# Performance work log

Measured on AMD Instinct MI355X. Metric: run time of the kernel, lower is better.

The kernel has to match this reference:

```python
import jax, jax.numpy as jnp
import numpy as np

B, S, H, NH, NL, G, D, A, T = 32, 512, 512, 8, 6, 8, 256, 18, 1024
HD = H // NH


def setup_inputs() -> dict:
    key = jax.random.key(0)
    ks = jax.random.split(key, 32)
    def n(k, shape, s=0.02):
        return jax.random.normal(k, shape, jnp.float32) * s
    return {
        'game_indices': jax.random.randint(ks[0], (B,), 0, G),
        'states': jax.random.normal(ks[1], (B, S, D), jnp.float32),
        'actions': jax.random.randint(ks[2], (B, S), 0, A),
        'returns_to_go': jax.random.normal(ks[3], (B, S), jnp.float32),
        'timesteps': jax.random.randint(ks[4], (B, S), 0, T),
        'attention_mask': jnp.ones((B, S), jnp.int32),
        'game_emb': n(ks[5], (G, H)),
        'obs_W': n(ks[6], (G, D, H)),
        'obs_b': n(ks[7], (G, H)),
        'obs_ln_g': jnp.ones((G, H), jnp.float32),
        'obs_ln_b': jnp.zeros((G, H), jnp.float32),
        'act_emb': n(ks[8], (G, A, H)),
        'ret_W': n(ks[9], (H,)),
        'ret_b': n(ks[10], (H,)),
        'time_emb': n(ks[11], (T, H)),
        'Wqkv': n(ks[12], (NL, 3 * H, H)),
        'bqkv': n(ks[13], (NL, 3 * H)),
        'Wo': n(ks[14], (NL, H, H)),
        'bo': n(ks[15], (NL, H)),
        'ln1_g': jnp.ones((NL, H), jnp.float32),
        'ln1_b': jnp.zeros((NL, H), jnp.float32),
        'W1': n(ks[16], (NL, 4 * H, H)),
        'b1': n(ks[17], (NL, 4 * H)),
        'W2': n(ks[18], (NL, H, 4 * H)),
        'b2': n(ks[19], (NL, H)),
        'ln2_g': jnp.ones((NL, H), jnp.float32),
        'ln2_b': jnp.zeros((NL, H), jnp.float32),
        'sh_W': n(ks[20], (G, H, D)),
        'sh_b': n(ks[21], (G, D)),
        'ah_W': n(ks[22], (G, H, A)),
        'ah_b': n(ks[23], (G, A)),
        'rh_W': n(ks[24], (H, 1)),
        'rh_b': n(ks[25], (1,)),
    }


def _ln(x, g, b, eps=1e-5):
    m = jnp.mean(x, -1, keepdims=True)
    v = jnp.mean((x - m) ** 2, -1, keepdims=True)
    return (x - m) / jnp.sqrt(v + eps) * g + b


def reference(game_indices, states, actions, returns_to_go, timesteps, attention_mask,
              game_emb, obs_W, obs_b, obs_ln_g, obs_ln_b, act_emb, ret_W, ret_b, time_emb,
              Wqkv, bqkv, Wo, bo, ln1_g, ln1_b, W1, b1, W2, b2, ln2_g, ln2_b,
              sh_W, sh_b, ah_W, ah_b, rh_W, rh_b):
    gi = game_indices
    g_emb = game_emb[gi][:, None, :]  # [B,1,H]
    # per-game routed observation embedding: Linear -> LayerNorm -> ReLU (grouped GEMM by game)
    se = jnp.einsum('bsd,bdh->bsh', states, obs_W[gi]) + obs_b[gi][:, None, :]
    se = jax.nn.relu(_ln(se, obs_ln_g[gi][:, None, :], obs_ln_b[gi][:, None, :]))
    # per-game routed action embedding table lookup
    ae = act_emb[gi[:, None], actions]  # [B,S,H]
    re = returns_to_go[..., None] * ret_W + ret_b  # Linear(1,H)
    te = time_emb[timesteps]
    x = se + ae + re + te + g_emb
    # key padding mask (src_key_padding_mask: True where attention_mask==0)
    bias = jnp.where((attention_mask == 0)[:, None, None, :], -1e9, 0.0)  # [B,1,1,S]
    scale = 1.0 / jnp.sqrt(jnp.asarray(HD, jnp.float32))
    for l in range(NL):  # post-norm TransformerEncoderLayer, relu, dropout=0 (eval)
        qkv = jnp.einsum('bsh,oh->bso', x, Wqkv[l]) + bqkv[l]
        q, k, v = jnp.split(qkv, 3, axis=-1)
        q = q.reshape(B, S, NH, HD).transpose(0, 2, 1, 3)
        k = k.reshape(B, S, NH, HD).transpose(0, 2, 1, 3)
        v = v.reshape(B, S, NH, HD).transpose(0, 2, 1, 3)
        scores = jnp.einsum('bhqd,bhkd->bhqk', q, k) * scale + bias
        attn = jnp.einsum('bhqk,bhkd->bhqd', jax.nn.softmax(scores, -1), v)
        attn = attn.transpose(0, 2, 1, 3).reshape(B, S, H)
        attn = jnp.einsum('bsh,oh->bso', attn, Wo[l]) + bo[l]
        x = _ln(x + attn, ln1_g[l], ln1_b[l])
        ff = jax.nn.relu(jnp.einsum('bsh,fh->bsf', x, W1[l]) + b1[l])
        ff = jnp.einsum('bsf,hf->bsh', ff, W2[l]) + b2[l]
        x = _ln(x + ff, ln2_g[l], ln2_b[l])
    # per-game routed prediction heads
    state_preds = jnp.einsum('bsh,bho->bso', x, sh_W[gi]) + sh_b[gi][:, None, :]
    action_preds = jnp.einsum('bsh,bho->bso', x, ah_W[gi]) + ah_b[gi][:, None, :]
    return_preds = x @ rh_W + rh_b
    return (state_preds, action_preds, return_preds)
```

## Files before the change

kernel.cpp:

```cpp
#include <hip/hip_runtime.h>

typedef __bf16 bf16x4 __attribute__((ext_vector_type(4)));
typedef __bf16 bf16x8 __attribute__((ext_vector_type(8)));
typedef float f32x4 __attribute__((ext_vector_type(4)));
typedef int int4v __attribute__((ext_vector_type(4)));

#define LOG2E 1.44269504088896340736f

typedef const __attribute__((address_space(1))) void gvoid_t;
typedef __attribute__((address_space(3))) void lvoid_t;


__global__ void cvt_f32_bf16(const float* __restrict__ src, __bf16* __restrict__ dst, int n4)
{
    int i = blockIdx.x * blockDim.x + threadIdx.x;
    if (i >= n4) return;
    f32x4 v = *reinterpret_cast<const f32x4*>(src + (size_t)i * 4);
    bf16x4 o;
    #pragma unroll
    for (int k = 0; k < 4; ++k) o[k] = (__bf16)v[k];
    *reinterpret_cast<bf16x4*>(dst + (size_t)i * 4) = o;
}

__global__ void transpose_cvt(const float* __restrict__ src, __bf16* __restrict__ dst, int R, int C)
{
    int m = blockIdx.y;
    int n = R * C;
    int i = blockIdx.x * 256 + threadIdx.x;
    if (i >= n) return;
    int c = i / R, r = i - c * R;
    dst[(size_t)m * n + i] = (__bf16)src[(size_t)m * n + (size_t)r * C + c];
}

__global__ void transpose_f32(const float* __restrict__ src, float* __restrict__ dst, int R, int C)
{
    int m = blockIdx.y;
    int n = R * C;
    int i = blockIdx.x * 256 + threadIdx.x;
    if (i >= n) return;
    int c = i / R, r = i - c * R;
    dst[(size_t)m * n + i] = src[(size_t)m * n + (size_t)r * C + c];
}

__global__ __launch_bounds__(256, 2)
void gemm_bt(const __bf16* __restrict__ A, size_t strideA,
             const __bf16* __restrict__ B, size_t strideB,
             const float* __restrict__ bias, int strideBias,
             float* Cf, __bf16* Cb, size_t strideC,
             const int* __restrict__ gidx,
             int K, int ldc, int relu)
{
    __shared__ __align__(16) char smem[16384];
    __bf16* lA  = (__bf16*)smem;
    __bf16* lB  = (__bf16*)(smem + 8192);
    __bf16* lCb = (__bf16*)smem;
    float*  lCf = (float*)smem;

    const int z = blockIdx.z;
    const int g = gidx ? gidx[z] : 0;
    const __bf16* Ab = A + (size_t)z * strideA;
    const __bf16* Bb = B + (size_t)g * strideB;

    const int nx = gridDim.x;
    const int nwg = nx * gridDim.y;
    int orig = blockIdx.y * nx + blockIdx.x;
    int wg = ((nwg & 7) == 0) ? ((orig & 7) * (nwg >> 3) + (orig >> 3)) : orig;
    const int bm = (wg / nx) * 128, bn = (wg % nx) * 128;

    const int t = threadIdx.x;
    const int w = t >> 6, lane = t & 63;
    const int wr = (w >> 1) * 64, wc = (w & 1) * 64;
    const int l16 = lane & 15, lk = lane >> 4;

    const int srow = lane >> 2;
    const int schunk = (lane & 3) ^ (srow & 3);
    const int ca = (lk ^ (l16 & 3)) * 8;

    f32x4 acc[4][4] = {};

    for (int kt = 0; kt < K; kt += 32) {
        __syncthreads();
        #pragma unroll
        for (int jj = 0; jj < 2; ++jj) {
            const __bf16* ga = Ab + (size_t)(bm + w * 32 + jj * 16 + srow) * K + kt + schunk * 8;
            __builtin_amdgcn_global_load_lds((gvoid_t*)ga, (lvoid_t*)&lA[(w * 32 + jj * 16) * 32], 16, 0, 0);
            const __bf16* gb = Bb + (size_t)(bn + w * 32 + jj * 16 + srow) * K + kt + schunk * 8;
            __builtin_amdgcn_global_load_lds((gvoid_t*)gb, (lvoid_t*)&lB[(w * 32 + jj * 16) * 32], 16, 0, 0);
        }
        __syncthreads();

        bf16x8 af[4], bfr[4];
        #pragma unroll
        for (int i = 0; i < 4; ++i) {
            af[i]  = *reinterpret_cast<const bf16x8*>(&lA[(wr + i * 16 + l16) * 32 + ca]);
            bfr[i] = *reinterpret_cast<const bf16x8*>(&lB[(wc + i * 16 + l16) * 32 + ca]);
        }
        #pragma unroll
        for (int mi = 0; mi < 4; ++mi)
            #pragma unroll
            for (int ni = 0; ni < 4; ++ni)
                acc[mi][ni] = __builtin_amdgcn_mfma_f32_16x16x32_bf16(af[mi], bfr[ni], acc[mi][ni], 0, 0, 0);
    }

    const float* biasb = bias ? bias + (size_t)g * strideBias : nullptr;

    if (Cb) {
        #pragma unroll
        for (int p = 0; p < 2; ++p) {
            __syncthreads();
            if (wr == p * 64) {
                #pragma unroll
                for (int ni = 0; ni < 4; ++ni) {
                    int col = wc + ni * 16 + l16;
                    float bv = biasb ? biasb[bn + col] : 0.f;
                    #pragma unroll
                    for (int mi = 0; mi < 4; ++mi)
                        #pragma unroll
                        for (int j = 0; j < 4; ++j) {
                            float v = acc[mi][ni][j] + bv;
                            if (relu) v = fmaxf(v, 0.f);
                            lCb[(mi * 16 + lk * 4 + j) * 128 + col] = (__bf16)v;
                        }
                }
            }
            __syncthreads();
            #pragma unroll
            for (int it = 0; it < 4; ++it) {
                int off = it * 2048 + t * 8;
                int rl = off >> 7, col = off & 127;
                *reinterpret_cast<int4v*>(Cb + (size_t)z * strideC + (size_t)(bm + p * 64 + rl) * ldc + bn + col) =
                    *reinterpret_cast<const int4v*>(&lCb[off]);
            }
        }
    } else {
        #pragma unroll
        for (int p = 0; p < 4; ++p) {
            __syncthreads();
            #pragma unroll
            for (int mi = 0; mi < 4; ++mi) {
                int rl = wr + mi * 16;
                if (rl >= p * 32 && rl < p * 32 + 32) {
                    #pragma unroll
                    for (int ni = 0; ni < 4; ++ni) {
                        int col = wc + ni * 16 + l16;
                        float bv = biasb ? biasb[bn + col] : 0.f;
                        #pragma unroll
                        for (int j = 0; j < 4; ++j) {
                            float v = acc[mi][ni][j] + bv;
                            if (relu) v = fmaxf(v, 0.f);
                            lCf[(rl - p * 32 + lk * 4 + j) * 128 + col] = v;
                        }
                    }
                }
            }
            __syncthreads();
            #pragma unroll
            for (int it = 0; it < 4; ++it) {
                int off = it * 1024 + t * 4;
                int rl = off >> 7, col = off & 127;
                *reinterpret_cast<f32x4*>(Cf + (size_t)z * strideC + (size_t)(bm + p * 32 + rl) * ldc + bn + col) =
                    *reinterpret_cast<const f32x4*>(&lCf[off]);
            }
        }
    }
}

__global__ __launch_bounds__(256, 2)
void attn_fwd(const __bf16* __restrict__ qkv, const int* __restrict__ mask,
              __bf16* __restrict__ out)
{
    __shared__ __bf16 lQ[128 * 64];
    __shared__ __bf16 lK[128 * 64];
    __shared__ __bf16 lVt[64 * 128];
    __shared__ float lMask[128];
    __shared__ __bf16 lP[4][32 * 32];

    const int b = blockIdx.z, h = blockIdx.y, q0 = blockIdx.x * 128;
    const int t = threadIdx.x, w = t >> 6, lane = t & 63;
    const int l16 = lane & 15, lk = lane >> 4;

    const __bf16* qbase = qkv + (size_t)b * 512 * 1536 + h * 64;
    const __bf16* kbase = qbase + 512;
    const __bf16* vbase = qbase + 1024;

    #pragma unroll
    for (int r = 0; r < 4; ++r) {
        int c = t + r * 256;
        int row = c >> 3, ch = c & 7;
        *reinterpret_cast<int4v*>(&lQ[row * 64 + ((ch ^ (row & 7)) * 8)]) =
            *reinterpret_cast<const int4v*>(qbase + (size_t)(q0 + row) * 1536 + ch * 8);
    }

    float m_run[2][4], l_run[2][4];
    f32x4 oacc[2][4] = {};
    #pragma unroll
    for (int mi = 0; mi < 2; ++mi)
        #pragma unroll
        for (int j = 0; j < 4; ++j) { m_run[mi][j] = -1e30f; l_run[mi][j] = 0.f; }

    for (int kt = 0; kt < 512; kt += 128) {
        __syncthreads();
        #pragma unroll
        for (int r = 0; r < 4; ++r) {
            int c = t + r * 256;
            int row = c >> 3, ch = c & 7;
            *reinterpret_cast<int4v*>(&lK[row * 64 + ((ch ^ (row & 7)) * 8)]) =
                *reinterpret_cast<const int4v*>(kbase + (size_t)(kt + row) * 1536 + ch * 8);
        }
        #pragma unroll
        for (int r = 0; r < 4; ++r) {
            int c = t + r * 256;
            int d = c & 63, kc8 = c >> 6;
            bf16x8 vv;
            #pragma unroll
            for (int i = 0; i < 8; ++i)
                vv[i] = vbase[(size_t)(kt + kc8 * 8 + i) * 1536 + d];
            *reinterpret_cast<bf16x8*>(&lVt[d * 128 + ((kc8 ^ (d & 7)) * 8)]) = vv;
        }
        if (t < 128) lMask[t] = (mask[b * 512 + kt + t] == 0) ? -1e9f : 0.f;
        __syncthreads();

        f32x4 sacc[2][8] = {};
        #pragma unroll
        for (int kc = 0; kc < 2; ++kc) {
            bf16x8 qf[2], kf[8];
            #pragma unroll
            for (int mi = 0; mi < 2; ++mi) {
                int row = w * 32 + mi * 16 + l16;
                qf[mi] = *reinterpret_cast<const bf16x8*>(&lQ[row * 64 + (((kc * 4 + lk) ^ (row & 7)) * 8)]);
            }
            #pragma unroll
            for (int ni = 0; ni < 8; ++ni) {
                int row = ni * 16 + l16;
                kf[ni] = *reinterpret_cast<const bf16x8*>(&lK[row * 64 + (((kc * 4 + lk) ^ (row & 7)) * 8)]);
            }
            #pragma unroll
            for (int mi = 0; mi < 2; ++mi)
                #pragma unroll
                for (int ni = 0; ni < 8; ++ni)
                    sacc[mi][ni] = __builtin_amdgcn_mfma_f32_16x16x32_bf16(qf[mi], kf[ni], sacc[mi][ni], 0, 0, 0);
        }

        #pragma unroll
        for (int mi = 0; mi < 2; ++mi) {
            float alpha[4];
            #pragma unroll
            for (int j = 0; j < 4; ++j) {
                float mx = -1e30f;
                #pragma unroll
                for (int ni = 0; ni < 8; ++ni) {
                    float sv = sacc[mi][ni][j] * 0.125f + lMask[ni * 16 + l16];
                    sacc[mi][ni][j] = sv;
                    mx = fmaxf(mx, sv);
                }
                #pragma unroll
                for (int d = 8; d >= 1; d >>= 1) mx = fmaxf(mx, __shfl_xor(mx, d));
                float mn = fmaxf(m_run[mi][j], mx);
                alpha[j] = exp2f((m_run[mi][j] - mn) * LOG2E);
                m_run[mi][j] = mn;
                float ps = 0.f;
                #pragma unroll
                for (int ni = 0; ni < 8; ++ni) {
                    float p = exp2f((sacc[mi][ni][j] - mn) * LOG2E);
                    sacc[mi][ni][j] = p;
                    ps += p;
                }
                l_run[mi][j] = l_run[mi][j] * alpha[j] + ps;
            }
            #pragma unroll
            for (int dn = 0; dn < 4; ++dn)
                #pragma unroll
                for (int j = 0; j < 4; ++j)
                    oacc[mi][dn][j] *= alpha[j];
        }

        __bf16* lp = &lP[w][0];
        #pragma unroll
        for (int kc = 0; kc < 4; ++kc) {
            #pragma unroll
            for (int mi = 0; mi < 2; ++mi)
                #pragma unroll
                for (int n2 = 0; n2 < 2; ++n2)
                    #pragma unroll
                    for (int j = 0; j < 4; ++j) {
                        int row = mi * 16 + lk * 4 + j;
                        lp[row * 32 + n2 * 16 + l16] = (__bf16)sacc[mi][kc * 2 + n2][j];
                    }
            bf16x8 pf[2], vf[4];
            #pragma unroll
            for (int mi = 0; mi < 2; ++mi)
                pf[mi] = *reinterpret_cast<const bf16x8*>(&lp[(mi * 16 + l16) * 32 + lk * 8]);
            #pragma unroll
            for (int dn = 0; dn < 4; ++dn) {
                int d = dn * 16 + l16;
                vf[dn] = *reinterpret_cast<const bf16x8*>(&lVt[d * 128 + (((kc * 4 + lk) ^ (d & 7)) * 8)]);
            }
            #pragma unroll
            for (int mi = 0; mi < 2; ++mi)
                #pragma unroll
                for (int dn = 0; dn < 4; ++dn)
                    oacc[mi][dn] = __builtin_amdgcn_mfma_f32_16x16x32_bf16(pf[mi], vf[dn], oacc[mi][dn], 0, 0, 0);
        }
    }

    #pragma unroll
    for (int mi = 0; mi < 2; ++mi) {
        float linv[4];
        #pragma unroll
        for (int j = 0; j < 4; ++j) {
            float s = l_run[mi][j];
            #pragma unroll
            for (int d = 8; d >= 1; d >>= 1) s += __shfl_xor(s, d);
            linv[j] = 1.f / s;
        }
        #pragma unroll
        for (int dn = 0; dn < 4; ++dn)
            #pragma unroll
            for (int j = 0; j < 4; ++j) {
                int row = q0 + w * 32 + mi * 16 + lk * 4 + j;
                int col = h * 64 + dn * 16 + l16;
                out[(size_t)(b * 512 + row) * 512 + col] = (__bf16)(oacc[mi][dn][j] * linv[j]);
            }
    }
}


__device__ __forceinline__ float wsum64(float v)
{
    #pragma unroll
    for (int d = 32; d >= 1; d >>= 1) v += __shfl_xor(v, d);
    return v;
}

__global__ __launch_bounds__(256)
void ln_fuse(const float* resid, const __bf16* __restrict__ proj,
             const float* __restrict__ gamma, const float* __restrict__ beta,
             float* xfo, __bf16* __restrict__ xbo)
{
    int tok = blockIdx.x * 4 + (threadIdx.x >> 6);
    int lane = threadIdx.x & 63;
    size_t base = (size_t)tok * 512 + lane * 8;
    float y[8];
    {
        f32x4 a0 = *reinterpret_cast<const f32x4*>(resid + base);
        f32x4 a1 = *reinterpret_cast<const f32x4*>(resid + base + 4);
        bf16x8 pv = *reinterpret_cast<const bf16x8*>(proj + base);
        #pragma unroll
        for (int i = 0; i < 4; ++i) { y[i] = a0[i] + (float)pv[i]; y[4 + i] = a1[i] + (float)pv[4 + i]; }
    }
    float s = 0.f;
    #pragma unroll
    for (int i = 0; i < 8; ++i) s += y[i];
    float mean = wsum64(s) * (1.f / 512.f);
    float v = 0.f;
    #pragma unroll
    for (int i = 0; i < 8; ++i) { float d = y[i] - mean; v += d * d; }
    float rstd = rsqrtf(wsum64(v) * (1.f / 512.f) + 1e-5f);
    int hh = lane * 8;
    f32x4 g0 = *reinterpret_cast<const f32x4*>(gamma + hh);
    f32x4 g1 = *reinterpret_cast<const f32x4*>(gamma + hh + 4);
    f32x4 b0 = *reinterpret_cast<const f32x4*>(beta + hh);
    f32x4 b1 = *reinterpret_cast<const f32x4*>(beta + hh + 4);
    f32x4 o0, o1;
    bf16x8 ob;
    #pragma unroll
    for (int i = 0; i < 4; ++i) {
        float t0 = (y[i] - mean) * rstd * g0[i] + b0[i];
        float t1 = (y[4 + i] - mean) * rstd * g1[i] + b1[i];
        o0[i] = t0; o1[i] = t1;
        ob[i] = (__bf16)t0; ob[4 + i] = (__bf16)t1;
    }
    *reinterpret_cast<f32x4*>(xfo + base) = o0;
    *reinterpret_cast<f32x4*>(xfo + base + 4) = o1;
    *reinterpret_cast<bf16x8*>(xbo + base) = ob;
}

__global__ __launch_bounds__(256)
void embed_fin(const __bf16* __restrict__ seraw, const int* __restrict__ gi,
               const int* __restrict__ actions, const float* __restrict__ rtg,
               const int* __restrict__ ts,
               const float* __restrict__ olg, const float* __restrict__ olb,
               const float* __restrict__ act_emb, const float* __restrict__ retW,
               const float* __restrict__ retb, const float* __restrict__ time_emb,
               const float* __restrict__ game_emb,
               float* __restrict__ xfo, __bf16* __restrict__ xbo)
{
    int tok = blockIdx.x * 4 + (threadIdx.x >> 6);
    int lane = threadIdx.x & 63;
    int b = tok >> 9;
    int g = gi[b];
    int a = actions[tok];
    int tt = ts[tok];
    float rv = rtg[tok];
    size_t base = (size_t)tok * 512 + lane * 8;
    int hh = lane * 8;

    float y[8];
    {
        bf16x8 a0 = *reinterpret_cast<const bf16x8*>(seraw + base);
        #pragma unroll
        for (int i = 0; i < 8; ++i) y[i] = (float)a0[i];
    }
    float s = 0.f;
    #pragma unroll
    for (int i = 0; i < 8; ++i) s += y[i];
    float mean = wsum64(s) * (1.f / 512.f);
    float v = 0.f;
    #pragma unroll
    for (int i = 0; i < 8; ++i) { float d = y[i] - mean; v += d * d; }
    float rstd = rsqrtf(wsum64(v) * (1.f / 512.f) + 1e-5f);

    const float* gp = olg + (size_t)g * 512 + hh;
    const float* bp = olb + (size_t)g * 512 + hh;
    const float* ap = act_emb + ((size_t)g * 18 + a) * 512 + hh;
    const float* tp = time_emb + (size_t)tt * 512 + hh;
    const float* ep = game_emb + (size_t)g * 512 + hh;
    const float* rwp = retW + hh;
    const float* rbp = retb + hh;

    f32x4 o0, o1;
    bf16x8 ob;
    #pragma unroll
    for (int half = 0; half < 2; ++half) {
        f32x4 gv = *reinterpret_cast<const f32x4*>(gp + half * 4);
        f32x4 bv = *reinterpret_cast<const f32x4*>(bp + half * 4);
        f32x4 av = *reinterpret_cast<const f32x4*>(ap + half * 4);
        f32x4 tv = *reinterpret_cast<const f32x4*>(tp + half * 4);
        f32x4 ev = *reinterpret_cast<const f32x4*>(ep + half * 4);
        f32x4 rw = *reinterpret_cast<const f32x4*>(rwp + half * 4);
        f32x4 rb = *reinterpret_cast<const f32x4*>(rbp + half * 4);
        #pragma unroll
        for (int i = 0; i < 4; ++i) {
            float n = (y[half * 4 + i] - mean) * rstd * gv[i] + bv[i];
            n = fmaxf(n, 0.f);
            float o = n + av[i] + rv * rw[i] + rb[i] + tv[i] + ev[i];
            if (half == 0) o0[i] = o; else o1[i] = o;
            ob[half * 4 + i] = (__bf16)o;
        }
    }
    *reinterpret_cast<f32x4*>(xfo + base) = o0;
    *reinterpret_cast<f32x4*>(xfo + base + 4) = o1;
    *reinterpret_cast<bf16x8*>(xbo + base) = ob;
}

__global__ __launch_bounds__(256)
void head_ar(const float* __restrict__ xf, const int* __restrict__ gi,
             const float* __restrict__ ahWt, const float* __restrict__ ah_b,
             const float* __restrict__ rhW, const float* __restrict__ rhb,
             float* __restrict__ outA, float* __restrict__ outR)
{
    int tok = blockIdx.x * 4 + (threadIdx.x >> 6);
    int lane = threadIdx.x & 63;
    int b = tok >> 9;
    int g = gi[b];
    size_t base = (size_t)tok * 512 + lane * 8;
    float x[8];
    {
        f32x4 a0 = *reinterpret_cast<const f32x4*>(xf + base);
        f32x4 a1 = *reinterpret_cast<const f32x4*>(xf + base + 4);
        #pragma unroll
        for (int i = 0; i < 4; ++i) { x[i] = a0[i]; x[4 + i] = a1[i]; }
    }
    #pragma unroll 1
    for (int a = 0; a < 18; ++a) {
        const float* wp = ahWt + ((size_t)g * 18 + a) * 512 + lane * 8;
        f32x4 w0 = *reinterpret_cast<const f32x4*>(wp);
        f32x4 w1 = *reinterpret_cast<const f32x4*>(wp + 4);
        float p = 0.f;
        #pragma unroll
        for (int i = 0; i < 4; ++i) { p += x[i] * w0[i]; p += x[4 + i] * w1[i]; }
        p = wsum64(p);
        if (lane == 0) outA[(size_t)tok * 18 + a] = p + ah_b[g * 18 + a];
    }
    {
        const float* wp = rhW + lane * 8;
        f32x4 w0 = *reinterpret_cast<const f32x4*>(wp);
        f32x4 w1 = *reinterpret_cast<const f32x4*>(wp + 4);
        float p = 0.f;
        #pragma unroll
        for (int i = 0; i < 4; ++i) { p += x[i] * w0[i]; p += x[4 + i] * w1[i]; }
        p = wsum64(p);
        if (lane == 0) outR[tok] = p + rhb[0];
    }
}


extern "C" void kernel_launch(void* const* d_in, const int* in_sizes, int n_in,
                              void* d_out, int out_size, void* d_ws, size_t ws_size,
                              hipStream_t stream)
{
    (void)in_sizes; (void)n_in; (void)out_size; (void)ws_size;

    const int*   gi       = (const int*)d_in[0];
    const float* states   = (const float*)d_in[1];
    const int*   actions  = (const int*)d_in[2];
    const float* rtg      = (const float*)d_in[3];
    const int*   ts       = (const int*)d_in[4];
    const int*   amask    = (const int*)d_in[5];
    const float* game_emb = (const float*)d_in[6];
    const float* obs_W    = (const float*)d_in[7];
    const float* obs_b    = (const float*)d_in[8];
    const float* obs_ln_g = (const float*)d_in[9];
    const float* obs_ln_b = (const float*)d_in[10];
    const float* act_emb  = (const float*)d_in[11];
    const float* ret_W    = (const float*)d_in[12];
    const float* ret_b    = (const float*)d_in[13];
    const float* time_emb = (const float*)d_in[14];
    const float* Wqkv     = (const float*)d_in[15];
    const float* bqkv     = (const float*)d_in[16];
    const float* Wo       = (const float*)d_in[17];
    const float* bo       = (const float*)d_in[18];
    const float* ln1_g    = (const float*)d_in[19];
    const float* ln1_b    = (const float*)d_in[20];
    const float* W1       = (const float*)d_in[21];
    const float* b1       = (const float*)d_in[22];
    const float* W2       = (const float*)d_in[23];
    const float* b2       = (const float*)d_in[24];
    const float* ln2_g    = (const float*)d_in[25];
    const float* ln2_b    = (const float*)d_in[26];
    const float* sh_W     = (const float*)d_in[27];
    const float* sh_b     = (const float*)d_in[28];
    const float* ah_W     = (const float*)d_in[29];
    const float* ah_b     = (const float*)d_in[30];
    const float* rh_W     = (const float*)d_in[31];
    const float* rh_b     = (const float*)d_in[32];

    char* wsb = (char*)d_ws;
    float*  xf      = (float*)(wsb + 0);
    __bf16* xb      = (__bf16*)(wsb + 33554432);
    __bf16* tmp     = (__bf16*)(wsb + 50331648);
    __bf16* qkvB    = (__bf16*)(wsb + 83886080);
    __bf16* ff1B    = qkvB;
    __bf16* statesB = qkvB;
    __bf16* obswB   = (__bf16*)(wsb + 83886080 + 8388608);
    __bf16* attnB   = (__bf16*)(wsb + 150994944);
    __bf16* wqkvB   = (__bf16*)(wsb + 167772160);
    __bf16* woB     = (__bf16*)(wsb + 177209344);
    __bf16* w1B     = (__bf16*)(wsb + 180355072);
    __bf16* w2B     = (__bf16*)(wsb + 192937984);
    __bf16* shwB    = (__bf16*)(wsb + 205520896);
    float*  ahwT    = (float*)(wsb + 207618048);

    cvt_f32_bf16<<<4608, 256, 0, stream>>>(Wqkv, wqkvB, 1179648);
    cvt_f32_bf16<<<1536, 256, 0, stream>>>(Wo, woB, 393216);
    cvt_f32_bf16<<<6144, 256, 0, stream>>>(W1, w1B, 1572864);
    cvt_f32_bf16<<<6144, 256, 0, stream>>>(W2, w2B, 1572864);
    cvt_f32_bf16<<<4096, 256, 0, stream>>>(states, statesB, 1048576);
    transpose_cvt<<<dim3(512, 8), 256, 0, stream>>>(obs_W, obswB, 256, 512);
    transpose_cvt<<<dim3(512, 8), 256, 0, stream>>>(sh_W, shwB, 512, 256);
    transpose_f32<<<dim3(36, 8), 256, 0, stream>>>(ah_W, ahwT, 512, 18);

    gemm_bt<<<dim3(4, 4, 32), 256, 0, stream>>>(
        statesB, (size_t)512 * 256, obswB, (size_t)512 * 256, obs_b, 512,
        nullptr, tmp, (size_t)512 * 512, gi, 256, 512, 0);
    embed_fin<<<4096, 256, 0, stream>>>(tmp, gi, actions, rtg, ts,
        obs_ln_g, obs_ln_b, act_emb, ret_W, ret_b, time_emb, game_emb, xf, xb);

    for (int l = 0; l < 6; ++l) {
        gemm_bt<<<dim3(12, 128, 1), 256, 0, stream>>>(
            xb, 0, wqkvB + (size_t)l * 1536 * 512, 0, bqkv + l * 1536, 0,
            nullptr, qkvB, 0, nullptr, 512, 1536, 0);
        attn_fwd<<<dim3(4, 8, 32), 256, 0, stream>>>(qkvB, amask, attnB);
        gemm_bt<<<dim3(4, 128, 1), 256, 0, stream>>>(
            attnB, 0, woB + (size_t)l * 512 * 512, 0, bo + l * 512, 0,
            nullptr, tmp, 0, nullptr, 512, 512, 0);
        ln_fuse<<<4096, 256, 0, stream>>>(xf, tmp, ln1_g + l * 512, ln1_b + l * 512, xf, xb);
        gemm_bt<<<dim3(16, 128, 1), 256, 0, stream>>>(
            xb, 0, w1B + (size_t)l * 2048 * 512, 0, b1 + l * 2048, 0,
            nullptr, ff1B, 0, nullptr, 512, 2048, 1);
        gemm_bt<<<dim3(4, 128, 1), 256, 0, stream>>>(
            ff1B, 0, w2B + (size_t)l * 512 * 2048, 0, b2 + l * 512, 0,
            nullptr, tmp, 0, nullptr, 2048, 512, 0);
        ln_fuse<<<4096, 256, 0, stream>>>(xf, tmp, ln2_g + l * 512, ln2_b + l * 512, xf, xb);
    }

    gemm_bt<<<dim3(2, 4, 32), 256, 0, stream>>>(
        xb, (size_t)512 * 512, shwB, (size_t)256 * 512, sh_b, 256,
        (float*)d_out, nullptr, (size_t)512 * 256, gi, 512, 256, 0);
    head_ar<<<4096, 256, 0, stream>>>(xf, gi, ahwT, ah_b, rh_W, rh_b,
        (float*)d_out + 4194304, (float*)d_out + 4489216);
}
```

Measured before the change: 1.635 ms.

## Double-buffer GEMM LDS tiles, keep Q in registers, skip unneeded softmax rescales

The GEMM now double-buffers its A/B LDS tiles so the next k-slice loads while MFMAs run, drops one barrier per iteration, and writes the output tile in fewer epilogue passes using the larger LDS. Occupancy hints go up for both kernels. The attention kernel keeps Q fragments in registers instead of LDS and folds scale times log2e into one FMA. It also skips the running-max rescale when no lane's max changed and swizzles the P scratch layout to cut bank conflicts. The costs are more LDS per GEMM block, which may conflict with the higher occupancy target, and more register pressure in attention.

```diff
diff --git a/kernel.cpp b/kernel.cpp
--- a/kernel.cpp
+++ b/kernel.cpp
@@ -6,6 +6,7 @@
 typedef int int4v __attribute__((ext_vector_type(4)));
 
 #define LOG2E 1.44269504088896340736f
+#define C1SM  0.18033688011112042592f
 
 typedef const __attribute__((address_space(1))) void gvoid_t;
 typedef __attribute__((address_space(3))) void lvoid_t;
@@ -42,7 +43,7 @@
     dst[(size_t)m * n + i] = src[(size_t)m * n + (size_t)r * C + c];
 }
 
-__global__ __launch_bounds__(256, 2)
+__global__ __launch_bounds__(256, 4)
 void gemm_bt(const __bf16* __restrict__ A, size_t strideA,
              const __bf16* __restrict__ B, size_t strideB,
              const float* __restrict__ bias, int strideBias,
@@ -50,9 +51,7 @@
              const int* __restrict__ gidx,
              int K, int ldc, int relu)
 {
-    __shared__ __align__(16) char smem[16384];
-    __bf16* lA  = (__bf16*)smem;
-    __bf16* lB  = (__bf16*)(smem + 8192);
+    __shared__ __align__(16) char smem[32768];
     __bf16* lCb = (__bf16*)smem;
     float*  lCf = (float*)smem;
 
@@ -78,36 +77,68 @@
 
     f32x4 acc[4][4] = {};
 
-    for (int kt = 0; kt < K; kt += 32) {
-        __syncthreads();
+    auto stage = [&](int buf, int kt) {
+        __bf16* la = (__bf16*)(smem + buf * 16384);
+        __bf16* lb = la + 4096;
         #pragma unroll
         for (int jj = 0; jj < 2; ++jj) {
             const __bf16* ga = Ab + (size_t)(bm + w * 32 + jj * 16 + srow) * K + kt + schunk * 8;
-            __builtin_amdgcn_global_load_lds((gvoid_t*)ga, (lvoid_t*)&lA[(w * 32 + jj * 16) * 32], 16, 0, 0);
+            __builtin_amdgcn_global_load_lds((gvoid_t*)ga, (lvoid_t*)&la[(w * 32 + jj * 16) * 32], 16, 0, 0);
             const __bf16* gb = Bb + (size_t)(bn + w * 32 + jj * 16 + srow) * K + kt + schunk * 8;
-            __builtin_amdgcn_global_load_lds((gvoid_t*)gb, (lvoid_t*)&lB[(w * 32 + jj * 16) * 32], 16, 0, 0);
-        }
-        __syncthreads();
-
+            __builtin_amdgcn_global_load_lds((gvoid_t*)gb, (lvoid_t*)&lb[(w * 32 + jj * 16) * 32], 16, 0, 0);
+        }
+    };
+
+    stage(0, 0);
+    __syncthreads();
+    int cur = 0;
+    for (int kt = 0; kt < K; kt += 32) {
+        if (kt + 32 < K) stage(cur ^ 1, kt + 32);
+        __bf16* la = (__bf16*)(smem + cur * 16384);
+        __bf16* lb = la + 4096;
         bf16x8 af[4], bfr[4];
         #pragma unroll
         for (int i = 0; i < 4; ++i) {
-            af[i]  = *reinterpret_cast<const bf16x8*>(&lA[(wr + i * 16 + l16) * 32 + ca]);
-            bfr[i] = *reinterpret_cast<const bf16x8*>(&lB[(wc + i * 16 + l16) * 32 + ca]);
+            af[i]  = *reinterpret_cast<const bf16x8*>(&la[(wr + i * 16 + l16) * 32 + ca]);
+            bfr[i] = *reinterpret_cast<const bf16x8*>(&lb[(wc + i * 16 + l16) * 32 + ca]);
         }
         #pragma unroll
         for (int mi = 0; mi < 4; ++mi)
             #pragma unroll
             for (int ni = 0; ni < 4; ++ni)
                 acc[mi][ni] = __builtin_amdgcn_mfma_f32_16x16x32_bf16(af[mi], bfr[ni], acc[mi][ni], 0, 0, 0);
+        __syncthreads();
+        cur ^= 1;
     }
 
     const float* biasb = bias ? bias + (size_t)g * strideBias : nullptr;
 
     if (Cb) {
         #pragma unroll
+        for (int ni = 0; ni < 4; ++ni) {
+            int col = wc + ni * 16 + l16;
+            float bv = biasb ? biasb[bn + col] : 0.f;
+            #pragma unroll
+            for (int mi = 0; mi < 4; ++mi)
+                #pragma unroll
+                for (int j = 0; j < 4; ++j) {
+                    float v = acc[mi][ni][j] + bv;
+                    if (relu) v = fmaxf(v, 0.f);
+                    lCb[(wr + mi * 16 + lk * 4 + j) * 128 + col] = (__bf16)v;
+                }
+        }
+        __syncthreads();
+        #pragma unroll
+        for (int it = 0; it < 8; ++it) {
+            int off = it * 2048 + t * 8;
+            int rl = off >> 7, col = off & 127;
+            *reinterpret_cast<int4v*>(Cb + (size_t)z * strideC + (size_t)(bm + rl) * ldc + bn + col) =
+                *reinterpret_cast<const int4v*>(&lCb[off]);
+        }
+    } else {
+        #pragma unroll
         for (int p = 0; p < 2; ++p) {
-            __syncthreads();
+            if (p) __syncthreads();
             if (wr == p * 64) {
                 #pragma unroll
                 for (int ni = 0; ni < 4; ++ni) {
@@ -119,61 +150,30 @@
                         for (int j = 0; j < 4; ++j) {
                             float v = acc[mi][ni][j] + bv;
                             if (relu) v = fmaxf(v, 0.f);
-                            lCb[(mi * 16 + lk * 4 + j) * 128 + col] = (__bf16)v;
+                            lCf[(mi * 16 + lk * 4 + j) * 128 + col] = v;
                         }
                 }
             }
             __syncthreads();
             #pragma unroll
-            for (int it = 0; it < 4; ++it) {
-                int off = it * 2048 + t * 8;
-                int rl = off >> 7, col = off & 127;
-                *reinterpret_cast<int4v*>(Cb + (size_t)z * strideC + (size_t)(bm + p * 64 + rl) * ldc + bn + col) =
-                    *reinterpret_cast<const int4v*>(&lCb[off]);
-            }
-        }
-    } else {
-        #pragma unroll
-        for (int p = 0; p < 4; ++p) {
-            __syncthreads();
-            #pragma unroll
-            for (int mi = 0; mi < 4; ++mi) {
-                int rl = wr + mi * 16;
-                if (rl >= p * 32 && rl < p * 32 + 32) {
-                    #pragma unroll
-                    for (int ni = 0; ni < 4; ++ni) {
-                        int col = wc + ni * 16 + l16;
-                        float bv = biasb ? biasb[bn + col] : 0.f;
-                        #pragma unroll
-                        for (int j = 0; j < 4; ++j) {
-                            float v = acc[mi][ni][j] + bv;
-                            if (relu) v = fmaxf(v, 0.f);
-                            lCf[(rl - p * 32 + lk * 4 + j) * 128 + col] = v;
-                        }
-                    }
-                }
-            }
-            __syncthreads();
-            #pragma unroll
-            for (int it = 0; it < 4; ++it) {
+            for (int it = 0; it < 8; ++it) {
                 int off = it * 1024 + t * 4;
                 int rl = off >> 7, col = off & 127;
-                *reinterpret_cast<f32x4*>(Cf + (size_t)z * strideC + (size_t)(bm + p * 32 + rl) * ldc + bn + col) =
+                *reinterpret_cast<f32x4*>(Cf + (size_t)z * strideC + (size_t)(bm + p * 64 + rl) * ldc + bn + col) =
                     *reinterpret_cast<const f32x4*>(&lCf[off]);
             }
         }
     }
 }
 
-__global__ __launch_bounds__(256, 2)
+__global__ __launch_bounds__(256, 3)
 void attn_fwd(const __bf16* __restrict__ qkv, const int* __restrict__ mask,
               __bf16* __restrict__ out)
 {
-    __shared__ __bf16 lQ[128 * 64];
     __shared__ __bf16 lK[128 * 64];
     __shared__ __bf16 lVt[64 * 128];
-    __shared__ float lMask[128];
     __shared__ __bf16 lP[4][32 * 32];
+    __shared__ float lM2[128];
 
     const int b = blockIdx.z, h = blockIdx.y, q0 = blockIdx.x * 128;
     const int t = threadIdx.x, w = t >> 6, lane = t & 63;
@@ -183,13 +183,14 @@
     const __bf16* kbase = qbase + 512;
     const __bf16* vbase = qbase + 1024;
 
-    #pragma unroll
-    for (int r = 0; r < 4; ++r) {
-        int c = t + r * 256;
-        int row = c >> 3, ch = c & 7;
-        *reinterpret_cast<int4v*>(&lQ[row * 64 + ((ch ^ (row & 7)) * 8)]) =
-            *reinterpret_cast<const int4v*>(qbase + (size_t)(q0 + row) * 1536 + ch * 8);
-    }
+    bf16x8 qfr[2][2];
+    #pragma unroll
+    for (int kc = 0; kc < 2; ++kc)
+        #pragma unroll
+        for (int mi = 0; mi < 2; ++mi) {
+            int row = q0 + w * 32 + mi * 16 + l16;
+            qfr[kc][mi] = *reinterpret_cast<const bf16x8*>(qbase + (size_t)row * 1536 + (kc * 4 + lk) * 8);
+        }
 
     float m_run[2][4], l_run[2][4];
     f32x4 oacc[2][4] = {};
@@ -217,18 +218,13 @@
                 vv[i] = vbase[(size_t)(kt + kc8 * 8 + i) * 1536 + d];
             *reinterpret_cast<bf16x8*>(&lVt[d * 128 + ((kc8 ^ (d & 7)) * 8)]) = vv;
         }
-        if (t < 128) lMask[t] = (mask[b * 512 + kt + t] == 0) ? -1e9f : 0.f;
+        if (t < 128) lM2[t] = (mask[b * 512 + kt + t] == 0) ? -2e9f : 0.f;
         __syncthreads();
 
         f32x4 sacc[2][8] = {};
         #pragma unroll
         for (int kc = 0; kc < 2; ++kc) {
-            bf16x8 qf[2], kf[8];
-            #pragma unroll
-            for (int mi = 0; mi < 2; ++mi) {
-                int row = w * 32 + mi * 16 + l16;
-                qf[mi] = *reinterpret_cast<const bf16x8*>(&lQ[row * 64 + (((kc * 4 + lk) ^ (row & 7)) * 8)]);
-            }
+            bf16x8 kf[8];
             #pragma unroll
             for (int ni = 0; ni < 8; ++ni) {
                 int row = ni * 16 + l16;
@@ -238,41 +234,58 @@
             for (int mi = 0; mi < 2; ++mi)
                 #pragma unroll
                 for (int ni = 0; ni < 8; ++ni)
-                    sacc[mi][ni] = __builtin_amdgcn_mfma_f32_16x16x32_bf16(qf[mi], kf[ni], sacc[mi][ni], 0, 0, 0);
-        }
-
-        #pragma unroll
-        for (int mi = 0; mi < 2; ++mi) {
-            float alpha[4];
+                    sacc[mi][ni] = __builtin_amdgcn_mfma_f32_16x16x32_bf16(qfr[kc][mi], kf[ni], sacc[mi][ni], 0, 0, 0);
+        }
+
+        float mnew[2][4];
+        bool changed = false;
+        #pragma unroll
+        for (int mi = 0; mi < 2; ++mi)
             #pragma unroll
             for (int j = 0; j < 4; ++j) {
-                float mx = -1e30f;
+                float mx = -3e38f;
                 #pragma unroll
                 for (int ni = 0; ni < 8; ++ni) {
-                    float sv = sacc[mi][ni][j] * 0.125f + lMask[ni * 16 + l16];
+                    float sv = fmaf(sacc[mi][ni][j], C1SM, lM2[ni * 16 + l16]);
                     sacc[mi][ni][j] = sv;
                     mx = fmaxf(mx, sv);
                 }
                 #pragma unroll
                 for (int d = 8; d >= 1; d >>= 1) mx = fmaxf(mx, __shfl_xor(mx, d));
                 float mn = fmaxf(m_run[mi][j], mx);
-                alpha[j] = exp2f((m_run[mi][j] - mn) * LOG2E);
-                m_run[mi][j] = mn;
+                mnew[mi][j] = mn;
+                changed |= (mn > m_run[mi][j]);
+            }
+        if (__any((int)changed)) {
+            #pragma unroll
+            for (int mi = 0; mi < 2; ++mi) {
+                float alpha[4];
+                #pragma unroll
+                for (int j = 0; j < 4; ++j) {
+                    alpha[j] = exp2f(m_run[mi][j] - mnew[mi][j]);
+                    l_run[mi][j] *= alpha[j];
+                }
+                #pragma unroll
+                for (int dn = 0; dn < 4; ++dn)
+                    #pragma unroll
+                    for (int j = 0; j < 4; ++j)
+                        oacc[mi][dn][j] *= alpha[j];
+            }
+        }
+        #pragma unroll
+        for (int mi = 0; mi < 2; ++mi)
+            #pragma unroll
+            for (int j = 0; j < 4; ++j) {
+                m_run[mi][j] = mnew[mi][j];
                 float ps = 0.f;
                 #pragma unroll
                 for (int ni = 0; ni < 8; ++ni) {
-                    float p = exp2f((sacc[mi][ni][j] - mn) * LOG2E);
+                    float p = exp2f(sacc[mi][ni][j] - mnew[mi][j]);
                     sacc[mi][ni][j] = p;
                     ps += p;
                 }
-                l_run[mi][j] = l_run[mi][j] * alpha[j] + ps;
-            }
-            #pragma unroll
-            for (int dn = 0; dn < 4; ++dn)
-                #pragma unroll
-                for (int j = 0; j < 4; ++j)
-                    oacc[mi][dn][j] *= alpha[j];
-        }
+                l_run[mi][j] += ps;
+            }
 
         __bf16* lp = &lP[w][0];
         #pragma unroll
@@ -284,12 +297,16 @@
                     #pragma unroll
                     for (int j = 0; j < 4; ++j) {
                         int row = mi * 16 + lk * 4 + j;
-                        lp[row * 32 + n2 * 16 + l16] = (__bf16)sacc[mi][kc * 2 + n2][j];
+                        int chw = (n2 * 2 + (l16 >> 3)) ^ lk;
+                        lp[row * 32 + chw * 8 + (l16 & 7)] = (__bf16)sacc[mi][kc * 2 + n2][j];
                     }
             bf16x8 pf[2], vf[4];
             #pragma unroll
-            for (int mi = 0; mi < 2; ++mi)
-                pf[mi] = *reinterpret_cast<const bf16x8*>(&lp[(mi * 16 + l16) * 32 + lk * 8]);
+            for (int mi = 0; mi < 2; ++mi) {
+                int rowr = mi * 16 + l16;
+                int chr = lk ^ ((l16 >> 2) & 3);
+                pf[mi] = *reinterpret_cast<const bf16x8*>(&lp[rowr * 32 + chr * 8]);
+            }
             #pragma unroll
             for (int dn = 0; dn < 4; ++dn) {
                 int d = dn * 16 + l16;
```

After: 1.886 ms. 1.15x slower.
